# Optimization experiments

Measured on AMD Instinct MI355X. Metric: run time of the kernel, lower is better.

## Reference

```python
import jax, jax.numpy as jnp
import numpy as np

EPS = 1.1920929e-07  # torch fp32 finfo eps used by F.rms_norm default

def rms_norm(x):
    return x * jax.lax.rsqrt(jnp.mean(jnp.square(x), axis=-1, keepdims=True) + EPS)

def setup_inputs() -> dict:
    key = jax.random.key(0)
    kx, kfc, kpr, krt = jax.random.split(key, 4)
    B, T, C, F = 4, 2048, 2048, 8192
    s = (3.0 ** 0.5) * C ** -0.5  # init scale used in init_weights
    x = jax.random.normal(kx, (B, T, C), dtype=jnp.float32)
    w_fc = jax.random.normal(kfc, (F, C), dtype=jnp.float32) * s
    w_proj = jax.random.normal(kpr, (C, F), dtype=jnp.float32) * (s * 0.1)
    w_router = jax.random.normal(krt, (1, C), dtype=jnp.float32) * 0.01  # router init std=0.01
    return {"x": x, "w_fc": w_fc, "w_proj": w_proj, "w_router": w_router}

def reference(x, w_fc, w_proj, w_router):
    # Router: (B,T,C) @ (C,1) -> (B,T) logits; STE mask (~0 or ~1 floats)
    logits = jnp.einsum('btc,oc->bto', x, w_router)[..., 0]  # (B,T)
    prob = jax.nn.sigmoid(logits)
    hard = (prob > 0.5).astype(x.dtype)
    mask_i = hard + prob - jax.lax.stop_gradient(prob)  # straight-through
    mask_bool = mask_i > 0.5  # (B,T)

    # Gated MLP (mixture-of-depth). The torch code gathers selected tokens,
    # runs the MLP on the compacted set, scatters into zeros, and multiplies
    # by mask_i. Mathematically identical dense form (honoring the mask):
    h = jnp.einsum('btc,fc->btf', rms_norm(x), w_fc)
    h = jnp.square(jax.nn.relu(h))  # relu(x)^2 activation
    mlp_out = jnp.einsum('btf,cf->btc', h, w_proj)
    gated = jnp.where(mask_bool[..., None], mlp_out * mask_i[..., None], 0.0)
    return x + gated
```

## Files before the change

kernel.cpp:

```cpp
#include <hip/hip_runtime.h>
#include <type_traits>
#include <utility>
#include <stdint.h>
#include <stddef.h>

#define TOKENS 8192
#define CDIM 2048
#define FDIM 8192
#define EPSV 1.1920929e-07f

typedef __attribute__((ext_vector_type(8))) short short8;
typedef __attribute__((ext_vector_type(8))) __bf16 bf16x8;
typedef __attribute__((ext_vector_type(4))) float floatx4;
typedef __attribute__((ext_vector_type(4))) float f32x4;
typedef __attribute__((ext_vector_type(2))) unsigned int u32x2;

template <typename V, typename = void> struct CanMfma : std::false_type {};
template <typename V>
struct CanMfma<V, std::void_t<decltype(__builtin_amdgcn_mfma_f32_16x16x32_bf16(
    std::declval<V>(), std::declval<V>(), std::declval<floatx4>(), 0, 0, 0))>>
    : std::true_type {};
using frag_t = std::conditional_t<CanMfma<short8>::value, short8, bf16x8>;

__device__ __forceinline__ floatx4 mfma_bf16(frag_t a, frag_t b, floatx4 c) {
    return __builtin_amdgcn_mfma_f32_16x16x32_bf16(a, b, c, 0, 0, 0);
}

__device__ __forceinline__ unsigned short f2bf(float f) {
    unsigned int u = __float_as_uint(f);
    u += 0x7fffu + ((u >> 16) & 1u);
    return (unsigned short)(u >> 16);
}

__global__ void zero_kernel(int* p) { if (threadIdx.x == 0) *p = 0; }


__global__ __launch_bounds__(256) void cvt2_kernel(
    const float* __restrict__ s1, unsigned short* __restrict__ d1,
    const float* __restrict__ s2, unsigned short* __restrict__ d2)
{
    const int NC1 = FDIM * (CDIM / 8);
    int i = blockIdx.x * 256 + threadIdx.x;
    const float* src; unsigned short* dst;
    int n, t, PK, K8;
    if (i < NC1) { src = s1; dst = d1; n = i >> 8; t = i & 255; PK = 32; K8 = 256; }
    else { i -= NC1; src = s2; dst = d2; n = i >> 10; t = i & 1023; PK = 128; K8 = 1024; }
    const int kt = t >> 3, q8 = t & 7;
    const int r = n & 127, ni = n >> 7;
    const float4* sp = (const float4*)src + ((size_t)n * K8 + t) * 2;
    float4 v0 = sp[0], v1 = sp[1];
    short8 o;
    o[0] = (short)f2bf(v0.x); o[1] = (short)f2bf(v0.y);
    o[2] = (short)f2bf(v0.z); o[3] = (short)f2bf(v0.w);
    o[4] = (short)f2bf(v1.x); o[5] = (short)f2bf(v1.y);
    o[6] = (short)f2bf(v1.z); o[7] = (short)f2bf(v1.w);
    size_t di = (((size_t)ni * PK + kt) * 128 + r) * 64 + (size_t)((q8 ^ (r & 7)) << 3);
    __builtin_nontemporal_store(o, (short8*)(dst + di));
}

__global__ __launch_bounds__(256) void router_kernel(
    const float* __restrict__ x, const float* __restrict__ wr,
    float* __restrict__ out, unsigned short* __restrict__ Xn,
    int* __restrict__ idx, float* __restrict__ mv, int* __restrict__ cnt)
{
    const int token = blockIdx.x;
    const int tid = threadIdx.x;
    const float4* xr = (const float4*)(x + (size_t)token * CDIM);
    const float4* w4 = (const float4*)wr;
    float4 a0 = xr[2 * tid];
    float4 a1 = xr[2 * tid + 1];
    float4 b0 = w4[2 * tid];
    float4 b1 = w4[2 * tid + 1];
    float ss = a0.x*a0.x + a0.y*a0.y + a0.z*a0.z + a0.w*a0.w
             + a1.x*a1.x + a1.y*a1.y + a1.z*a1.z + a1.w*a1.w;
    float dt = a0.x*b0.x + a0.y*b0.y + a0.z*b0.z + a0.w*b0.w
             + a1.x*b1.x + a1.y*b1.y + a1.z*b1.z + a1.w*b1.w;
    #pragma unroll
    for (int off = 32; off > 0; off >>= 1) {
        ss += __shfl_down(ss, off);
        dt += __shfl_down(dt, off);
    }
    __shared__ float red_ss[4], red_dt[4];
    __shared__ float s_rms;
    __shared__ int s_pos;
    const int wave = tid >> 6;
    if ((tid & 63) == 0) { red_ss[wave] = ss; red_dt[wave] = dt; }
    __syncthreads();
    if (tid == 0) {
        float S = red_ss[0] + red_ss[1] + red_ss[2] + red_ss[3];
        float D = red_dt[0] + red_dt[1] + red_dt[2] + red_dt[3];
        float prob = 1.0f / (1.0f + expf(-D));
        s_rms = 1.0f / sqrtf(S * (1.0f / (float)CDIM) + EPSV);
        int pos = -1;
        if (prob > 0.5f) {
            pos = atomicAdd(cnt, 1);
            idx[pos] = token;
            mv[pos] = (1.0f + prob) - prob;
        }
        s_pos = pos;
    }
    __syncthreads();
    const float rms = s_rms;
    const int pos = s_pos;
    float* op = out + (size_t)token * CDIM;
    if (pos < 0) {
        f32x4 r0 = {a0.x, a0.y, a0.z, a0.w};
        f32x4 r1 = {a1.x, a1.y, a1.z, a1.w};
        __builtin_nontemporal_store(r0, (f32x4*)(op + tid * 8));
        __builtin_nontemporal_store(r1, (f32x4*)(op + tid * 8 + 4));
    } else {
        const int kt = tid >> 3, q8 = tid & 7;
        const int r = pos & 127, mi = pos >> 7;
        short8 o;
        o[0] = (short)f2bf(a0.x * rms); o[1] = (short)f2bf(a0.y * rms);
        o[2] = (short)f2bf(a0.z * rms); o[3] = (short)f2bf(a0.w * rms);
        o[4] = (short)f2bf(a1.x * rms); o[5] = (short)f2bf(a1.y * rms);
        o[6] = (short)f2bf(a1.z * rms); o[7] = (short)f2bf(a1.w * rms);
        size_t di = (((size_t)mi * 32 + kt) * 128 + r) * 64 + (size_t)((q8 ^ (r & 7)) << 3);
        __builtin_nontemporal_store(o, (short8*)(Xn + di));
    }
}

template <int K, int MODE, int LDO, int KSPLIT>
__global__ __launch_bounds__(256) void gemm_bt(
    const unsigned short* __restrict__ A,
    const unsigned short* __restrict__ B,
    unsigned short* __restrict__ Hout,
    float* __restrict__ out,
    const float* __restrict__ xin,
    const int* __restrict__ idx,
    const float* __restrict__ mv,
    const int* __restrict__ cntp)
{
    const int cnt = *cntp;
    const int bid = blockIdx.y * 64 + blockIdx.x;
    const int s = bid >> 6;
    const int w = bid & 63;
    const int mi = (s & 7) * 8 + (w & 7);
    const int ni = (s >> 3) * 8 + (w >> 3);
    const int m0 = mi * 128;
    if (m0 >= cnt) return;
    const int n0 = ni * 128;
    const int k0 = (int)blockIdx.z * (K / KSPLIT);

    __shared__ alignas(16) unsigned short lA[128 * 64];
    __shared__ alignas(16) unsigned short lB[128 * 64];

    const int tid = threadIdx.x;
    const int wave = tid >> 6;
    const int lane = tid & 63;
    const int wm = (wave >> 1) * 64;
    const int wn = (wave & 1) * 64;
    const int quad = lane >> 4;
    const int l16 = lane & 15;

    constexpr int PK = K / 64;
    const unsigned short* aq = A + ((size_t)mi * PK + (k0 >> 6)) * 8192 + (size_t)tid * 8;
    const unsigned short* bq = B + ((size_t)ni * PK + (k0 >> 6)) * 8192 + (size_t)tid * 8;

    floatx4 acc[4][4] = {};

    for (int kt = 0; kt < K / (64 * KSPLIT); ++kt) {
        #pragma unroll
        for (int p = 0; p < 4; ++p) {
            __builtin_amdgcn_global_load_lds(
                (__attribute__((address_space(1))) void*)(aq + p * 2048),
                (__attribute__((address_space(3))) void*)&lA[(p * 256 + wave * 64) * 8],
                16, 0, 0);
            __builtin_amdgcn_global_load_lds(
                (__attribute__((address_space(1))) void*)(bq + p * 2048),
                (__attribute__((address_space(3))) void*)&lB[(p * 256 + wave * 64) * 8],
                16, 0, 0);
        }
        aq += 8192;
        bq += 8192;
        __syncthreads();
        #pragma unroll
        for (int st = 0; st < 2; ++st) {
            frag_t af[4], bfv[4];
            #pragma unroll
            for (int t = 0; t < 4; ++t) {
                const int ra = wm + t * 16 + l16;
                const int ca = ((st * 4 + quad) ^ (ra & 7)) * 8;
                af[t] = *(const frag_t*)&lA[ra * 64 + ca];
                const int rb = wn + t * 16 + l16;
                const int cb = ((st * 4 + quad) ^ (rb & 7)) * 8;
                bfv[t] = *(const frag_t*)&lB[rb * 64 + cb];
            }
            #pragma unroll
            for (int tm = 0; tm < 4; ++tm)
                #pragma unroll
                for (int tn = 0; tn < 4; ++tn)
                    acc[tm][tn] = mfma_bf16(af[tm], bfv[tn], acc[tm][tn]);
        }
        __syncthreads();
    }

    if (MODE == 1) {
        constexpr int PKH = LDO / 64;
        #pragma unroll
        for (int tm = 0; tm < 4; ++tm) {
            const int rbase = wm + tm * 16 + quad * 4;
            #pragma unroll
            for (int tn = 0; tn < 4; ++tn) {
                const int gn = n0 + wn + tn * 16 + l16;
                const int kt = gn >> 6, q8 = (gn >> 3) & 7, e = gn & 7;
                #pragma unroll
                for (int v = 0; v < 4; ++v) {
                    const int r = rbase + v;
                    float h = fmaxf(acc[tm][tn][v], 0.0f);
                    size_t di = (((size_t)mi * PKH + kt) * 128 + r) * 64
                              + (size_t)((q8 ^ (r & 7)) << 3) + e;
                    __builtin_nontemporal_store(f2bf(h * h), &Hout[di]);
                }
            }
        }
    } else {
        #pragma unroll
        for (int tm = 0; tm < 4; ++tm) {
            const int gmb = m0 + wm + tm * 16 + quad * 4;
            #pragma unroll
            for (int v = 0; v < 4; ++v) {
                const int gm = gmb + v;
                if (gm < cnt) {
                    const int token = idx[gm];
                    const float scale = mv[gm];
                    const float* xrow = xin + (size_t)token * LDO;
                    float* orow = out + (size_t)token * LDO;
                    #pragma unroll
                    for (int tn = 0; tn < 4; ++tn) {
                        const int gn = n0 + wn + tn * 16 + l16;
                        float r = xrow[gn] + scale * acc[tm][tn][v];
                        __builtin_nontemporal_store(r, &orow[gn]);
                    }
                }
            }
        }
    }
}

extern "C" void kernel_launch(void* const* d_in, const int* in_sizes, int n_in,
                              void* d_out, int out_size, void* d_ws, size_t ws_size,
                              hipStream_t stream)
{
    const float* x   = (const float*)d_in[0];
    const float* wfc = (const float*)d_in[1];
    const float* wpr = (const float*)d_in[2];
    const float* wrt = (const float*)d_in[3];
    float* out = (float*)d_out;

    char* ws = (char*)d_ws;
    int*   cnt = (int*)ws;
    int*   idx = (int*)(ws + 256);
    float* mv  = (float*)(ws + 256 + 32768);
    unsigned short* Xn  = (unsigned short*)(ws + 65792);
    unsigned short* Wfc = (unsigned short*)(ws + 65792 + 33554432ULL);
    unsigned short* Wpr = (unsigned short*)(ws + 65792 + 67108864ULL);
    unsigned short* H   = (unsigned short*)(ws + 65792 + 100663296ULL);

    const int nchunks = FDIM * (CDIM / 8) + CDIM * (FDIM / 8);
    zero_kernel<<<1, 64, 0, stream>>>(cnt);
    cvt2_kernel<<<nchunks / 256, 256, 0, stream>>>(wfc, Wfc, wpr, Wpr);
    router_kernel<<<TOKENS, 256, 0, stream>>>(x, wrt, out, Xn, idx, mv, cnt);
    gemm_bt<CDIM, 1, FDIM, 1><<<dim3(64, FDIM / 128), 256, 0, stream>>>(
        Xn, Wfc, H, nullptr, nullptr, nullptr, nullptr, cnt);
    gemm_bt<FDIM, 2, CDIM, 1><<<dim3(64, CDIM / 128), 256, 0, stream>>>(
        H, Wpr, nullptr, out, x, idx, mv, cnt);
}
```

Before: 753.5 us.

## Convert GEMMs to persistent XCD-sliced kernels with 512-thread blocks

Replaces the fixed 2D grid with a persistent grid of 512 blocks. Each block loops over output tiles, and tiles are partitioned by XCD (blockIdx & 7) into N-column slices so that blocks sharing B tiles stay on the same chiplet's L2. Blocks grow to 8 waves, each computing 64x32 instead of 64x64, with occupancy hinted at 4 blocks per CU. The goal is to avoid launching and early-exiting idle blocks when few tokens are selected and to improve L2 locality. The cost is a single-buffered LDS loop with full barriers per K-step and less MFMA work per wave between syncs.

```diff
diff --git a/kernel.cpp b/kernel.cpp
--- a/kernel.cpp
+++ b/kernel.cpp
@@ -121,8 +121,8 @@
     }
 }
 
-template <int K, int MODE, int LDO, int KSPLIT>
-__global__ __launch_bounds__(256) void gemm_bt(
+template <int K, int MODE, int LDO, int NP>
+__global__ __launch_bounds__(512, 4) void gemm_bt(
     const unsigned short* __restrict__ A,
     const unsigned short* __restrict__ B,
     unsigned short* __restrict__ Hout,
@@ -133,105 +133,119 @@
     const int* __restrict__ cntp)
 {
     const int cnt = *cntp;
-    const int bid = blockIdx.y * 64 + blockIdx.x;
-    const int s = bid >> 6;
-    const int w = bid & 63;
-    const int mi = (s & 7) * 8 + (w & 7);
-    const int ni = (s >> 3) * 8 + (w >> 3);
-    const int m0 = mi * 128;
-    if (m0 >= cnt) return;
-    const int n0 = ni * 128;
-    const int k0 = (int)blockIdx.z * (K / KSPLIT);
-
-    __shared__ alignas(16) unsigned short lA[128 * 64];
-    __shared__ alignas(16) unsigned short lB[128 * 64];
+    const int mp = (cnt + 127) >> 7;
+    const int xcd = blockIdx.x & 7;
+    const int wix = blockIdx.x >> 3;
+    constexpr int NPX = NP / 8;
+    const int tiles_slice = mp * NPX;
+    const int crew = (int)gridDim.x >> 3;
 
     const int tid = threadIdx.x;
     const int wave = tid >> 6;
     const int lane = tid & 63;
-    const int wm = (wave >> 1) * 64;
-    const int wn = (wave & 1) * 64;
+    const int wm = (wave >> 2) * 64;
+    const int wn = (wave & 3) * 32;
     const int quad = lane >> 4;
     const int l16 = lane & 15;
 
+    __shared__ alignas(16) unsigned short lA[128 * 64];
+    __shared__ alignas(16) unsigned short lB[128 * 64];
+
     constexpr int PK = K / 64;
-    const unsigned short* aq = A + ((size_t)mi * PK + (k0 >> 6)) * 8192 + (size_t)tid * 8;
-    const unsigned short* bq = B + ((size_t)ni * PK + (k0 >> 6)) * 8192 + (size_t)tid * 8;
-
-    floatx4 acc[4][4] = {};
-
-    for (int kt = 0; kt < K / (64 * KSPLIT); ++kt) {
-        #pragma unroll
-        for (int p = 0; p < 4; ++p) {
-            __builtin_amdgcn_global_load_lds(
-                (__attribute__((address_space(1))) void*)(aq + p * 2048),
-                (__attribute__((address_space(3))) void*)&lA[(p * 256 + wave * 64) * 8],
-                16, 0, 0);
-            __builtin_amdgcn_global_load_lds(
-                (__attribute__((address_space(1))) void*)(bq + p * 2048),
-                (__attribute__((address_space(3))) void*)&lB[(p * 256 + wave * 64) * 8],
-                16, 0, 0);
+    constexpr int NT = K / 64;
+
+    for (int t = wix; t < tiles_slice; t += crew) {
+        const int mi = t % mp;
+        const int ni = xcd * NPX + t / mp;
+        const int m0 = mi * 128;
+        const int n0 = ni * 128;
+
+        const unsigned short* aq = A + (size_t)mi * PK * 8192 + (size_t)tid * 8;
+        const unsigned short* bq = B + (size_t)ni * PK * 8192 + (size_t)tid * 8;
+
+        floatx4 acc[4][2] = {};
+
+        for (int kt = 0; kt < NT; ++kt) {
+            __builtin_amdgcn_global_load_lds(
+                (__attribute__((address_space(1))) void*)aq,
+                (__attribute__((address_space(3))) void*)&lA[(size_t)tid * 8],
+                16, 0, 0);
+            __builtin_amdgcn_global_load_lds(
+                (__attribute__((address_space(1))) void*)(aq + 512 * 8),
+                (__attribute__((address_space(3))) void*)&lA[((size_t)tid + 512) * 8],
+                16, 0, 0);
+            __builtin_amdgcn_global_load_lds(
+                (__attribute__((address_space(1))) void*)bq,
+                (__attribute__((address_space(3))) void*)&lB[(size_t)tid * 8],
+                16, 0, 0);
+            __builtin_amdgcn_global_load_lds(
+                (__attribute__((address_space(1))) void*)(bq + 512 * 8),
+                (__attribute__((address_space(3))) void*)&lB[((size_t)tid + 512) * 8],
+                16, 0, 0);
+            aq += 8192;
+            bq += 8192;
+            __syncthreads();
+            #pragma unroll
+            for (int st = 0; st < 2; ++st) {
+                frag_t af[4], bfv[2];
+                #pragma unroll
+                for (int tt = 0; tt < 4; ++tt) {
+                    const int ra = wm + tt * 16 + l16;
+                    const int ca = ((st * 4 + quad) ^ (ra & 7)) * 8;
+                    af[tt] = *(const frag_t*)&lA[ra * 64 + ca];
+                }
+                #pragma unroll
+                for (int tt = 0; tt < 2; ++tt) {
+                    const int rb = wn + tt * 16 + l16;
+                    const int cb = ((st * 4 + quad) ^ (rb & 7)) * 8;
+                    bfv[tt] = *(const frag_t*)&lB[rb * 64 + cb];
+                }
+                #pragma unroll
+                for (int tm = 0; tm < 4; ++tm)
+                    #pragma unroll
+                    for (int tn = 0; tn < 2; ++tn)
+                        acc[tm][tn] = mfma_bf16(af[tm], bfv[tn], acc[tm][tn]);
+            }
+            __syncthreads();
         }
-        aq += 8192;
-        bq += 8192;
-        __syncthreads();
-        #pragma unroll
-        for (int st = 0; st < 2; ++st) {
-            frag_t af[4], bfv[4];
+
+        if (MODE == 1) {
+            constexpr int PKH = LDO / 64;
             #pragma unroll
-            for (int t = 0; t < 4; ++t) {
-                const int ra = wm + t * 16 + l16;
-                const int ca = ((st * 4 + quad) ^ (ra & 7)) * 8;
-                af[t] = *(const frag_t*)&lA[ra * 64 + ca];
-                const int rb = wn + t * 16 + l16;
-                const int cb = ((st * 4 + quad) ^ (rb & 7)) * 8;
-                bfv[t] = *(const frag_t*)&lB[rb * 64 + cb];
+            for (int tm = 0; tm < 4; ++tm) {
+                const int rbase = wm + tm * 16 + quad * 4;
+                #pragma unroll
+                for (int tn = 0; tn < 2; ++tn) {
+                    const int gn = n0 + wn + tn * 16 + l16;
+                    const int kt = gn >> 6, q8 = (gn >> 3) & 7, e = gn & 7;
+                    #pragma unroll
+                    for (int v = 0; v < 4; ++v) {
+                        const int r = rbase + v;
+                        float h = fmaxf(acc[tm][tn][v], 0.0f);
+                        size_t di = (((size_t)mi * PKH + kt) * 128 + r) * 64
+                                  + (size_t)((q8 ^ (r & 7)) << 3) + e;
+                        __builtin_nontemporal_store(f2bf(h * h), &Hout[di]);
+                    }
+                }
             }
+        } else {
             #pragma unroll
-            for (int tm = 0; tm < 4; ++tm)
-                #pragma unroll
-                for (int tn = 0; tn < 4; ++tn)
-                    acc[tm][tn] = mfma_bf16(af[tm], bfv[tn], acc[tm][tn]);
-        }
-        __syncthreads();
-    }
-
-    if (MODE == 1) {
-        constexpr int PKH = LDO / 64;
-        #pragma unroll
-        for (int tm = 0; tm < 4; ++tm) {
-            const int rbase = wm + tm * 16 + quad * 4;
-            #pragma unroll
-            for (int tn = 0; tn < 4; ++tn) {
-                const int gn = n0 + wn + tn * 16 + l16;
-                const int kt = gn >> 6, q8 = (gn >> 3) & 7, e = gn & 7;
+            for (int tm = 0; tm < 4; ++tm) {
+                const int gmb = m0 + wm + tm * 16 + quad * 4;
                 #pragma unroll
                 for (int v = 0; v < 4; ++v) {
-                    const int r = rbase + v;
-                    float h = fmaxf(acc[tm][tn][v], 0.0f);
-                    size_t di = (((size_t)mi * PKH + kt) * 128 + r) * 64
-                              + (size_t)((q8 ^ (r & 7)) << 3) + e;
-                    __builtin_nontemporal_store(f2bf(h * h), &Hout[di]);
-                }
-            }
-        }
-    } else {
-        #pragma unroll
-        for (int tm = 0; tm < 4; ++tm) {
-            const int gmb = m0 + wm + tm * 16 + quad * 4;
-            #pragma unroll
-            for (int v = 0; v < 4; ++v) {
-                const int gm = gmb + v;
-                if (gm < cnt) {
-                    const int token = idx[gm];
-                    const float scale = mv[gm];
-                    const float* xrow = xin + (size_t)token * LDO;
-                    float* orow = out + (size_t)token * LDO;
-                    #pragma unroll
-                    for (int tn = 0; tn < 4; ++tn) {
-                        const int gn = n0 + wn + tn * 16 + l16;
-                        float r = xrow[gn] + scale * acc[tm][tn][v];
-                        __builtin_nontemporal_store(r, &orow[gn]);
+                    const int gm = gmb + v;
+                    if (gm < cnt) {
+                        const int token = idx[gm];
+                        const float scale = mv[gm];
+                        const float* xrow = xin + (size_t)token * LDO;
+                        float* orow = out + (size_t)token * LDO;
+                        #pragma unroll
+                        for (int tn = 0; tn < 2; ++tn) {
+                            const int gn = n0 + wn + tn * 16 + l16;
+                            float r = xrow[gn] + scale * acc[tm][tn][v];
+                            __builtin_nontemporal_store(r, &orow[gn]);
+                        }
                     }
                 }
             }
@@ -262,8 +276,8 @@
     zero_kernel<<<1, 64, 0, stream>>>(cnt);
     cvt2_kernel<<<nchunks / 256, 256, 0, stream>>>(wfc, Wfc, wpr, Wpr);
     router_kernel<<<TOKENS, 256, 0, stream>>>(x, wrt, out, Xn, idx, mv, cnt);
-    gemm_bt<CDIM, 1, FDIM, 1><<<dim3(64, FDIM / 128), 256, 0, stream>>>(
+    gemm_bt<CDIM, 1, FDIM, FDIM / 128><<<512, 512, 0, stream>>>(
         Xn, Wfc, H, nullptr, nullptr, nullptr, nullptr, cnt);
-    gemm_bt<FDIM, 2, CDIM, 1><<<dim3(64, CDIM / 128), 256, 0, stream>>>(
+    gemm_bt<FDIM, 2, CDIM, CDIM / 128><<<512, 512, 0, stream>>>(
         H, Wpr, nullptr, out, x, idx, mv, cnt);
 }
```

Measured after the change: 748.3 us. No clear change (-0.7%).

## Use 256x256 tiles with register-staged double-buffered LDS and split-K atomics

Applied to the files above, without the earlier changes.

Grows GEMM tiles from 128x128 to 256x256 with 512 threads and 8 waves. Global loads now go through registers into a double-buffered 128KB dynamic LDS region, so the next tile's load overlaps the current compute with one barrier per step. The router now writes x to every output row so the second GEMM can split K in two and accumulate with float atomicAdd instead of reading x. This adds atomic traffic and ordering nondeterminism, and the large LDS footprint limits occupancy.

```diff
diff --git a/kernel.cpp b/kernel.cpp
--- a/kernel.cpp
+++ b/kernel.cpp
@@ -103,12 +103,11 @@
     const float rms = s_rms;
     const int pos = s_pos;
     float* op = out + (size_t)token * CDIM;
-    if (pos < 0) {
-        f32x4 r0 = {a0.x, a0.y, a0.z, a0.w};
-        f32x4 r1 = {a1.x, a1.y, a1.z, a1.w};
-        __builtin_nontemporal_store(r0, (f32x4*)(op + tid * 8));
-        __builtin_nontemporal_store(r1, (f32x4*)(op + tid * 8 + 4));
-    } else {
+    f32x4 r0 = {a0.x, a0.y, a0.z, a0.w};
+    f32x4 r1 = {a1.x, a1.y, a1.z, a1.w};
+    __builtin_nontemporal_store(r0, (f32x4*)(op + tid * 8));
+    __builtin_nontemporal_store(r1, (f32x4*)(op + tid * 8 + 4));
+    if (pos >= 0) {
         const int kt = tid >> 3, q8 = tid & 7;
         const int r = pos & 127, mi = pos >> 7;
         short8 o;
@@ -122,102 +121,136 @@
 }
 
 template <int K, int MODE, int LDO, int KSPLIT>
-__global__ __launch_bounds__(256) void gemm_bt(
+__global__ __launch_bounds__(512, 2) void gemm_bt(
     const unsigned short* __restrict__ A,
     const unsigned short* __restrict__ B,
     unsigned short* __restrict__ Hout,
     float* __restrict__ out,
-    const float* __restrict__ xin,
     const int* __restrict__ idx,
     const float* __restrict__ mv,
     const int* __restrict__ cntp)
 {
     const int cnt = *cntp;
-    const int bid = blockIdx.y * 64 + blockIdx.x;
+    const int bid = blockIdx.y * 32 + blockIdx.x;
     const int s = bid >> 6;
     const int w = bid & 63;
-    const int mi = (s & 7) * 8 + (w & 7);
-    const int ni = (s >> 3) * 8 + (w >> 3);
-    const int m0 = mi * 128;
+    const int mi = (s & 3) * 8 + (w & 7);
+    const int ni = (s >> 2) * 8 + (w >> 3);
+    const int m0 = mi * 256;
     if (m0 >= cnt) return;
-    const int n0 = ni * 128;
+    const int n0 = ni * 256;
     const int k0 = (int)blockIdx.z * (K / KSPLIT);
 
-    __shared__ alignas(16) unsigned short lA[128 * 64];
-    __shared__ alignas(16) unsigned short lB[128 * 64];
+    extern __shared__ unsigned short lds[];
 
     const int tid = threadIdx.x;
     const int wave = tid >> 6;
     const int lane = tid & 63;
-    const int wm = (wave >> 1) * 64;
-    const int wn = (wave & 1) * 64;
+    const int wm = (wave >> 2) * 128;
+    const int wn = (wave & 3) * 64;
     const int quad = lane >> 4;
     const int l16 = lane & 15;
 
     constexpr int PK = K / 64;
-    const unsigned short* aq = A + ((size_t)mi * PK + (k0 >> 6)) * 8192 + (size_t)tid * 8;
-    const unsigned short* bq = B + ((size_t)ni * PK + (k0 >> 6)) * 8192 + (size_t)tid * 8;
-
-    floatx4 acc[4][4] = {};
-
-    for (int kt = 0; kt < K / (64 * KSPLIT); ++kt) {
-        #pragma unroll
-        for (int p = 0; p < 4; ++p) {
-            __builtin_amdgcn_global_load_lds(
-                (__attribute__((address_space(1))) void*)(aq + p * 2048),
-                (__attribute__((address_space(3))) void*)&lA[(p * 256 + wave * 64) * 8],
-                16, 0, 0);
-            __builtin_amdgcn_global_load_lds(
-                (__attribute__((address_space(1))) void*)(bq + p * 2048),
-                (__attribute__((address_space(3))) void*)&lB[(p * 256 + wave * 64) * 8],
-                16, 0, 0);
-        }
-        aq += 8192;
-        bq += 8192;
-        __syncthreads();
+    constexpr int NT = K / (64 * KSPLIT);
+
+    const unsigned short* aSrc[4];
+    const unsigned short* bSrc[4];
+    #pragma unroll
+    for (int j = 0; j < 4; ++j) {
+        const int c = tid + j * 512;
+        aSrc[j] = A + ((size_t)(2 * mi + (c >> 10)) * PK + (k0 >> 6)) * 8192
+                    + (size_t)(c & 1023) * 8;
+        bSrc[j] = B + ((size_t)(2 * ni + (c >> 10)) * PK + (k0 >> 6)) * 8192
+                    + (size_t)(c & 1023) * 8;
+    }
+
+    short8 ar[4], br[4];
+
+    auto LOAD = [&](int kt) {
+        #pragma unroll
+        for (int j = 0; j < 4; ++j) {
+            ar[j] = *(const short8*)(aSrc[j] + (size_t)kt * 8192);
+            br[j] = *(const short8*)(bSrc[j] + (size_t)kt * 8192);
+        }
+    };
+    auto WRITE = [&](int buf) {
+        unsigned short* base = &lds[buf * 32768];
+        #pragma unroll
+        for (int j = 0; j < 4; ++j) {
+            const int c = tid + j * 512;
+            *(short8*)&base[(size_t)c * 8] = ar[j];
+            *(short8*)&base[16384 + (size_t)c * 8] = br[j];
+        }
+    };
+
+    floatx4 acc[8][4] = {};
+
+    auto COMPUTE = [&](int buf) {
+        const unsigned short* bA = &lds[buf * 32768];
+        const unsigned short* bB = &lds[buf * 32768 + 16384];
         #pragma unroll
         for (int st = 0; st < 2; ++st) {
-            frag_t af[4], bfv[4];
-            #pragma unroll
-            for (int t = 0; t < 4; ++t) {
-                const int ra = wm + t * 16 + l16;
-                const int ca = ((st * 4 + quad) ^ (ra & 7)) * 8;
-                af[t] = *(const frag_t*)&lA[ra * 64 + ca];
-                const int rb = wn + t * 16 + l16;
-                const int cb = ((st * 4 + quad) ^ (rb & 7)) * 8;
-                bfv[t] = *(const frag_t*)&lB[rb * 64 + cb];
+            frag_t af[8], bf[4];
+            #pragma unroll
+            for (int m = 0; m < 8; ++m) {
+                const int ra = wm + m * 16 + l16;
+                af[m] = *(const frag_t*)&bA[(ra >> 7) * 8192 + (ra & 127) * 64
+                                            + (((st * 4 + quad) ^ (ra & 7)) << 3)];
             }
             #pragma unroll
-            for (int tm = 0; tm < 4; ++tm)
+            for (int n = 0; n < 4; ++n) {
+                const int rb = wn + n * 16 + l16;
+                bf[n] = *(const frag_t*)&bB[(rb >> 7) * 8192 + (rb & 127) * 64
+                                            + (((st * 4 + quad) ^ (rb & 7)) << 3)];
+            }
+            #pragma unroll
+            for (int m = 0; m < 8; ++m)
                 #pragma unroll
-                for (int tn = 0; tn < 4; ++tn)
-                    acc[tm][tn] = mfma_bf16(af[tm], bfv[tn], acc[tm][tn]);
-        }
-        __syncthreads();
+                for (int n = 0; n < 4; ++n)
+                    acc[m][n] = mfma_bf16(af[m], bf[n], acc[m][n]);
+        }
+    };
+
+    LOAD(0);
+    WRITE(0);
+    if (NT > 1) LOAD(1);
+    asm volatile("s_waitcnt lgkmcnt(0)" ::: "memory");
+    __builtin_amdgcn_s_barrier();
+    asm volatile("" ::: "memory");
+
+    for (int kt = 0; kt < NT; ++kt) {
+        if (kt + 1 < NT) WRITE((kt + 1) & 1);
+        if (kt + 2 < NT) LOAD(kt + 2);
+        COMPUTE(kt & 1);
+        asm volatile("s_waitcnt lgkmcnt(0)" ::: "memory");
+        __builtin_amdgcn_s_barrier();
+        asm volatile("" ::: "memory");
     }
 
     if (MODE == 1) {
         constexpr int PKH = LDO / 64;
         #pragma unroll
-        for (int tm = 0; tm < 4; ++tm) {
+        for (int tm = 0; tm < 8; ++tm) {
             const int rbase = wm + tm * 16 + quad * 4;
             #pragma unroll
             for (int tn = 0; tn < 4; ++tn) {
                 const int gn = n0 + wn + tn * 16 + l16;
-                const int kt = gn >> 6, q8 = (gn >> 3) & 7, e = gn & 7;
+                const int kth = gn >> 6, q8 = (gn >> 3) & 7, e = gn & 7;
                 #pragma unroll
                 for (int v = 0; v < 4; ++v) {
                     const int r = rbase + v;
+                    const int gr = m0 + r;
                     float h = fmaxf(acc[tm][tn][v], 0.0f);
-                    size_t di = (((size_t)mi * PKH + kt) * 128 + r) * 64
-                              + (size_t)((q8 ^ (r & 7)) << 3) + e;
+                    size_t di = (((size_t)(gr >> 7) * PKH + kth) * 128 + (gr & 127)) * 64
+                              + (size_t)((q8 ^ (gr & 7)) << 3) + e;
                     __builtin_nontemporal_store(f2bf(h * h), &Hout[di]);
                 }
             }
         }
     } else {
         #pragma unroll
-        for (int tm = 0; tm < 4; ++tm) {
+        for (int tm = 0; tm < 8; ++tm) {
             const int gmb = m0 + wm + tm * 16 + quad * 4;
             #pragma unroll
             for (int v = 0; v < 4; ++v) {
@@ -225,13 +258,11 @@
                 if (gm < cnt) {
                     const int token = idx[gm];
                     const float scale = mv[gm];
-                    const float* xrow = xin + (size_t)token * LDO;
                     float* orow = out + (size_t)token * LDO;
                     #pragma unroll
                     for (int tn = 0; tn < 4; ++tn) {
                         const int gn = n0 + wn + tn * 16 + l16;
-                        float r = xrow[gn] + scale * acc[tm][tn][v];
-                        __builtin_nontemporal_store(r, &orow[gn]);
+                        atomicAdd(&orow[gn], scale * acc[tm][tn][v]);
                     }
                 }
             }
@@ -262,8 +293,8 @@
     zero_kernel<<<1, 64, 0, stream>>>(cnt);
     cvt2_kernel<<<nchunks / 256, 256, 0, stream>>>(wfc, Wfc, wpr, Wpr);
     router_kernel<<<TOKENS, 256, 0, stream>>>(x, wrt, out, Xn, idx, mv, cnt);
-    gemm_bt<CDIM, 1, FDIM, 1><<<dim3(64, FDIM / 128), 256, 0, stream>>>(
-        Xn, Wfc, H, nullptr, nullptr, nullptr, nullptr, cnt);
-    gemm_bt<FDIM, 2, CDIM, 1><<<dim3(64, CDIM / 128), 256, 0, stream>>>(
-        H, Wpr, nullptr, out, x, idx, mv, cnt);
-}
+    gemm_bt<CDIM, 1, FDIM, 1><<<dim3(32, FDIM / 256), 512, 131072, stream>>>(
+        Xn, Wfc, H, nullptr, nullptr, nullptr, cnt);
+    gemm_bt<FDIM, 2, CDIM, 2><<<dim3(32, CDIM / 256, 2), 512, 131072, stream>>>(
+        H, Wpr, nullptr, out, idx, mv, cnt);
+}
```

Result: faster. 719.6 us (-4.5%).
